# Kernel optimization log

Hardware: AMD Instinct MI355X
Metric: run time of the kernel (lower is better)

Reference implementation:

```python
import jax, jax.numpy as jnp
import numpy as np

B, K, D = 65536, 1024, 256
COMMITMENT_COST = 0.25


def setup_inputs() -> dict:
    key = jax.random.key(0)
    kz, kw = jax.random.split(key)
    z = jax.random.normal(kz, (B, D), dtype=jnp.float32)
    # torch init: uniform_(-1/num_embeddings, 1/num_embeddings)
    weight = jax.random.uniform(kw, (K, D), dtype=jnp.float32,
                                minval=-1.0 / K, maxval=1.0 / K)
    return {"z": z, "weight": weight}


def reference(z, weight):
    # squared L2 distances via expansion: ||z||^2 - 2 z.e + ||e||^2  -> [B, K]
    dists = (jnp.sum(z * z, axis=1, keepdims=True)
             - 2.0 * (z @ weight.T)
             + jnp.sum(weight * weight, axis=1))
    indices = jnp.argmin(dists, axis=1)          # [B]
    z_q = weight[indices]                         # [B, D] gather

    sg_z = jax.lax.stop_gradient(z)
    mse = jnp.mean((z_q - sg_z) ** 2)
    commitment_loss = COMMITMENT_COST * mse      # F.mse_loss(z.detach(), z_q)
    vq_loss = mse + commitment_loss              # F.mse_loss(z_q, z.detach()) + commitment

    # straight-through estimator
    z_q_st = z + jax.lax.stop_gradient(z_q - z)
    return z_q_st, vq_loss, indices
```

## Files before the change

### kernel.cpp

```cpp
#include <hip/hip_runtime.h>
#include <math.h>

#define B_N 65536
#define K_N 1024
#define D_N 256
#define CAPW 512
#define NWV 8

typedef __attribute__((ext_vector_type(8))) short bf16x8;
typedef __attribute__((ext_vector_type(4))) float f32x4;

__device__ __forceinline__ unsigned short f2bf(float f) {
    unsigned u = __float_as_uint(f);
    return (unsigned short)((u + 0x7FFFu + ((u >> 16) & 1u)) >> 16);
}
__device__ __forceinline__ unsigned encf(float f) {
    unsigned u = __float_as_uint(f);
    return u ^ ((unsigned)((int)u >> 31) | 0x80000000u);
}
__device__ __forceinline__ float decf(unsigned e) {
    unsigned u = (e & 0x80000000u) ? (e ^ 0x80000000u) : ~e;
    return __uint_as_float(u);
}
__device__ __forceinline__ void gload_lds16(const void* g, void* l) {
    __builtin_amdgcn_global_load_lds(
        (const __attribute__((address_space(1))) unsigned int*)g,
        (__attribute__((address_space(3))) unsigned int*)l, 16, 0, 0);
}

__device__ __forceinline__ float chain_dot(const float* __restrict__ zp,
                                           const float* __restrict__ wp) {
    float acc = 0.0f;
    #pragma unroll 1
    for (int j = 0; j < 64; ++j) {
        float4 za = *reinterpret_cast<const float4*>(zp + (j << 2));
        float4 wa = *reinterpret_cast<const float4*>(wp + (j << 2));
        acc = fmaf(za.x, wa.x, acc);
        acc = fmaf(za.y, wa.y, acc);
        acc = fmaf(za.z, wa.z, acc);
        acc = fmaf(za.w, wa.w, acc);
    }
    return acc;
}

__device__ __forceinline__ int pA(int i, int k) {
    return ((i + k) & 15) - 7 + 9 * ((k >> 4) & 1);
}
__device__ __forceinline__ int pB(int j, int k) {
    return ((j + 3 * k) & 15) - 7 + 5 * ((k >> 4) & 1);
}

__global__ void mfma_probe_kernel(int* __restrict__ flag) {
    const int l = threadIdx.x & 63;
    const int c15 = l & 15, g = l >> 4;
    bf16x8 afr[8], bfr[8];
    #pragma unroll
    for (int m = 0; m < 8; ++m)
        #pragma unroll
        for (int e = 0; e < 8; ++e) {
            const int k = m * 32 + g * 8 + e;
            afr[m][e] = (short)f2bf((float)pA(c15, k));
            bfr[m][e] = (short)f2bf((float)pB(c15, k));
        }
    f32x4 acc = {0.f, 0.f, 0.f, 0.f};
    #pragma unroll
    for (int m = 0; m < 8; ++m)
        acc = __builtin_amdgcn_mfma_f32_16x16x32_bf16(afr[m], bfr[m], acc, 0, 0, 0);
    int h1 = 1, h2 = 1;
    #pragma unroll 1
    for (int reg = 0; reg < 4; ++reg) {
        const int q = 4 * g + reg;
        int e1 = 0, e2 = 0;
        for (int k = 0; k < 32; ++k) {
            e1 += pA(q, k) * pB(c15, k);
            e2 += pA(c15, k) * pB(q, k);
        }
        e1 *= 8; e2 *= 8;
        if (acc[reg] != (float)e1) h1 = 0;
        if (acc[reg] != (float)e2) h2 = 0;
    }
    h1 = __all(h1); h2 = __all(h2);
    if (threadIdx.x == 0) *flag = h1 ? 0 : (h2 ? 1 : 2);
}

__global__ void wprep_kernel(const float* __restrict__ w,
                             float* __restrict__ ww,
                             unsigned short* __restrict__ wb) {
    int wave = (int)((blockIdx.x * blockDim.x + threadIdx.x) >> 6);
    int lane = threadIdx.x & 63;
    if (wave >= K_N) return;
    const float4 v = *reinterpret_cast<const float4*>(w + ((size_t)wave << 8) + (lane << 2));
    float s = v.x * v.x + v.y * v.y + v.z * v.z + v.w * v.w;
    #pragma unroll
    for (int off = 32; off; off >>= 1) s += __shfl_xor(s, off, 64);
    if (lane == 0) ww[wave] = s;
    ushort4 b;
    b.x = f2bf(v.x); b.y = f2bf(v.y); b.z = f2bf(v.z); b.w = f2bf(v.w);
    const int mp = lane >> 3;
    const int gp = (lane >> 1) & 3;
    const int hp = (wave >> 4) & 1;
    const size_t off_b = (size_t)(wave >> 5) * 16384
        + (size_t)(((hp * 8 + mp) * 64 + gp * 16 + (wave & 15)) * 16)
        + (size_t)((lane & 1) * 8);
    *reinterpret_cast<ushort4*>((char*)wb + off_b) = b;
}

__global__ __launch_bounds__(512, 4)
void vq_mfma_kernel(const float* __restrict__ z, const float* __restrict__ w,
                    const unsigned short* __restrict__ wb,
                    const float* __restrict__ ww,
                    const int* __restrict__ flagp,
                    float* __restrict__ zq_out,
                    float* __restrict__ idxf_out,
                    double* __restrict__ partial) {
    __shared__ alignas(16) short wbl[3][8192];
    __shared__ float wwlds[1024];
    __shared__ unsigned short rc[NWV][CAPW];
    __shared__ unsigned short dqv[NWV][CAPW];
    __shared__ float zz_l[NWV][16], band_l[NWV][16], thrm[NWV][16];
    __shared__ unsigned rowminU[NWV][16];
    __shared__ unsigned long long bestk[NWV][16];
    __shared__ double wsum[NWV];

    const int tid = threadIdx.x;
    const int wv = tid >> 6, l = tid & 63;
    const int c15 = l & 15, g = l >> 4;
    const int b0 = blockIdx.x << 7;
    const int rbase = b0 + (wv << 4);
    const int flag = flagp[0];
    const bool fb0 = !(flag == 0 || flag == 1);

#define STAGE(T, BUF) do {                                                    \
        const char* _s = (const char*)wb + (size_t)(T) * 16384 + tid * 16;    \
        char* _d = (char*)&wbl[BUF][0] + tid * 16;                            \
        gload_lds16(_s,         _d);                                          \
        gload_lds16(_s + 8192,  _d + 8192);                                   \
    } while (0)

    STAGE(0, 0);

    if (l < 16) {
        rowminU[wv][l] = 0xFFFFFFFFu;
        bestk[wv][l]   = ~0ull;
    }
    reinterpret_cast<float2*>(wwlds)[tid] = reinterpret_cast<const float2*>(ww)[tid];

    bool fbw = fb0;
    int n = 0;

    int ml[4], cl[4];
    #pragma unroll
    for (int reg = 0; reg < 4; ++reg) {
        if (flag == 1) { ml[reg] = c15;          cl[reg] = 4 * g + reg; }
        else           { ml[reg] = 4 * g + reg;  cl[reg] = c15;         }
    }

    bf16x8 afr[8];
    {
        const float* zr = z + ((size_t)(rbase + c15) << 8) + (g << 3);
        float s = 0.0f, a = 0.0f;
        #pragma unroll
        for (int m = 0; m < 8; ++m) {
            float4 lo = *reinterpret_cast<const float4*>(zr + (m << 5));
            float4 hi = *reinterpret_cast<const float4*>(zr + (m << 5) + 4);
            s += lo.x * lo.x + lo.y * lo.y + lo.z * lo.z + lo.w * lo.w;
            s += hi.x * hi.x + hi.y * hi.y + hi.z * hi.z + hi.w * hi.w;
            a += fabsf(lo.x) + fabsf(lo.y) + fabsf(lo.z) + fabsf(lo.w);
            a += fabsf(hi.x) + fabsf(hi.y) + fabsf(hi.z) + fabsf(hi.w);
            bf16x8 f;
            f[0] = (short)f2bf(lo.x); f[1] = (short)f2bf(lo.y);
            f[2] = (short)f2bf(lo.z); f[3] = (short)f2bf(lo.w);
            f[4] = (short)f2bf(hi.x); f[5] = (short)f2bf(hi.y);
            f[6] = (short)f2bf(hi.z); f[7] = (short)f2bf(hi.w);
            afr[m] = f;
        }
        s += __shfl_xor(s, 16, 64);
        s += __shfl_xor(s, 32, 64);
        a += __shfl_xor(a, 16, 64);
        a += __shfl_xor(a, 32, 64);
        if (g == 0) {
            zz_l[wv][c15]   = s;
            band_l[wv][c15] = a * 2.0e-5f + 1.0e-3f;
        }
    }

    STAGE(1, 1);

    __syncthreads();

    float zzv[4], bdv[4];
    #pragma unroll
    for (int reg = 0; reg < 4; ++reg) {
        zzv[reg] = zz_l[wv][ml[reg]];
        bdv[reg] = band_l[wv][ml[reg]];
    }

    float runmin[4] = {INFINITY, INFINITY, INFINITY, INFINITY};
    int base = 0;

#define ITER(C, CUR0, CUR1, PRV0, PRV1) do {                                  \
    if ((C) <= 32) {                                                          \
        if ((C) <= 30) {                                                      \
            const int _st = ((C) + 2 <= 31) ? ((C) + 2) : 0;                  \
            STAGE(_st, ((C) + 2) % 3);                                        \
        }                                                                     \
        const short* _sb = wbl[(C) % 3];                                      \
        CUR0 = (f32x4){0.f, 0.f, 0.f, 0.f};                                   \
        CUR1 = (f32x4){0.f, 0.f, 0.f, 0.f};                                   \
        _Pragma("unroll")                                                     \
        for (int m = 0; m < 8; ++m) {                                         \
            bf16x8 _b = *reinterpret_cast<const bf16x8*>(                     \
                &_sb[(m << 9) + (l << 3)]);                                   \
            CUR0 = __builtin_amdgcn_mfma_f32_16x16x32_bf16(afr[m], _b, CUR0, 0, 0, 0); \
        }                                                                     \
        _Pragma("unroll")                                                     \
        for (int m = 0; m < 8; ++m) {                                         \
            bf16x8 _b = *reinterpret_cast<const bf16x8*>(                     \
                &_sb[((8 + m) << 9) + (l << 3)]);                             \
            CUR1 = __builtin_amdgcn_mfma_f32_16x16x32_bf16(afr[m], _b, CUR1, 0, 0, 0); \
        }                                                                     \
    }                                                                         \
    if ((C) >= 1) {                                                           \
        const int _tc = ((C) <= 32) ? ((C) - 1) : 0;                          \
        const bool _docol = ((C) >= 2);                                       \
        const bool _dofm = ((C) <= 32);                                       \
        _Pragma("unroll")                                                     \
        for (int h = 0; h < 2; ++h) {                                         \
            const f32x4 _acc = h ? (PRV1) : (PRV0);                           \
            _Pragma("unroll")                                                 \
            for (int reg = 0; reg < 4; ++reg) {                               \
                const int _code = (_tc << 5) + (h << 4) + cl[reg];            \
                const float _dist = (zzv[reg] - 2.0f * _acc[reg]) + wwlds[_code]; \
                if (_docol) {                                                 \
                    const bool _pred = (_dist <= runmin[reg] + bdv[reg]);     \
                    const unsigned long long _mask = __ballot(_pred);         \
                    if (_mask) {                                              \
                        if (_pred) {                                          \
                            const int _slot = base + (int)__popcll(_mask & ((1ull << l) - 1ull)); \
                            if (_slot < CAPW) {                               \
                                rc[wv][_slot] = (unsigned short)((ml[reg] << 10) | _code); \
                                union { _Float16 h16; unsigned short u; } _cv; \
                                _cv.h16 = (_Float16)(_dist - zzv[reg]);       \
                                dqv[wv][_slot] = _cv.u;                       \
                            }                                                 \
                        }                                                     \
                        base += (int)__popcll(_mask);                         \
                    }                                                         \
                }                                                             \
                if (_dofm) runmin[reg] = fminf(runmin[reg], _dist);           \
            }                                                                 \
        }                                                                     \
        if (_dofm) {                                                          \
            if (flag == 1) {                                                  \
                _Pragma("unroll")                                             \
                for (int reg = 0; reg < 4; ++reg) {                           \
                    runmin[reg] = fminf(runmin[reg], __shfl_xor(runmin[reg], 16, 64)); \
                    runmin[reg] = fminf(runmin[reg], __shfl_xor(runmin[reg], 32, 64)); \
                }                                                             \
            } else {                                                          \
                _Pragma("unroll")                                             \
                for (int reg = 0; reg < 4; ++reg) {                           \
                    runmin[reg] = fminf(runmin[reg], __shfl_xor(runmin[reg], 1, 64)); \
                    runmin[reg] = fminf(runmin[reg], __shfl_xor(runmin[reg], 2, 64)); \
                    runmin[reg] = fminf(runmin[reg], __shfl_xor(runmin[reg], 4, 64)); \
                    runmin[reg] = fminf(runmin[reg], __shfl_xor(runmin[reg], 8, 64)); \
                }                                                             \
            }                                                                 \
        }                                                                     \
    }                                                                         \
    if ((C) <= 31) {                                                          \
        if ((C) <= 30) { asm volatile("s_waitcnt vmcnt(2) lgkmcnt(0)" ::: "memory"); } \
        else           { asm volatile("s_waitcnt vmcnt(0) lgkmcnt(0)" ::: "memory"); } \
        __builtin_amdgcn_sched_barrier(0);                                    \
        __builtin_amdgcn_s_barrier();                                         \
        __builtin_amdgcn_sched_barrier(0);                                    \
    }                                                                         \
} while (0)

    if (!fb0) {
        f32x4 aA0 = {0.f, 0.f, 0.f, 0.f}, aA1 = {0.f, 0.f, 0.f, 0.f};
        f32x4 aB0 = {0.f, 0.f, 0.f, 0.f}, aB1 = {0.f, 0.f, 0.f, 0.f};
        #pragma unroll 1
        for (int c = 0; c < 34; c += 2) {
            ITER(c,     aA0, aA1, aB0, aB1);
            ITER(c + 1, aB0, aB1, aA0, aA1);
        }

        n = base;
        if (n > CAPW) fbw = true;

        #pragma unroll
        for (int reg = 0; reg < 4; ++reg)
            atomicMin(&rowminU[wv][ml[reg]], encf(runmin[reg]));
        if (l < 16)
            thrm[wv][l] = (decf(rowminU[wv][l]) + band_l[wv][l]) - zz_l[wv][l] + 4.0e-4f;
    }
#undef ITER
#undef STAGE

    if (!fbw) {
        int viol = 0;
        #pragma unroll 1
        for (int i = l; i < n; i += 64) {
            const int e = rc[wv][i];
            const int m = e >> 10, code = e & 1023;
            union { _Float16 h16; unsigned short u; } cv;
            cv.u = dqv[wv][i];
            const float dval = (float)cv.h16;
            if (dval <= thrm[wv][m]) {
                const float dot = chain_dot(z + ((size_t)(rbase + m) << 8),
                                            w + ((size_t)code << 8));
                const float dist = (zz_l[wv][m] - 2.0f * dot) + wwlds[code];
                if (fabsf((dval + zz_l[wv][m]) - dist) > band_l[wv][m] + 4.0e-4f)
                    viol = 1;
                atomicMin(&bestk[wv][m],
                          ((unsigned long long)encf(dist) << 32) | (unsigned)code);
            }
        }
        if (__any(viol)) fbw = true;
    }
    if (fbw) {
        #pragma unroll 1
        for (int m = 0; m < 16; ++m) {
            const float zzm = zz_l[wv][m];
            const float* zp = z + ((size_t)(rbase + m) << 8);
            for (int code = l; code < 1024; code += 64) {
                const float dist = (zzm - 2.0f * chain_dot(zp, w + ((size_t)code << 8)))
                                 + wwlds[code];
                atomicMin(&bestk[wv][m],
                          ((unsigned long long)encf(dist) << 32) | (unsigned)code);
            }
        }
    }

    if (l < 16) {
        const int code = (int)(unsigned)(bestk[wv][l] & 0xFFFFFFFFull);
        idxf_out[rbase + l] = (float)code;
    }

    int codes[16];
    #pragma unroll
    for (int rr = 0; rr < 16; ++rr)
        codes[rr] = (int)(unsigned)(bestk[wv][rr] & 0xFFFFFFFFull);
    #pragma unroll 4
    for (int rr = 0; rr < 16; ++rr) {
        const float4 wv4 = *reinterpret_cast<const float4*>(
            w + ((size_t)codes[rr] << 8) + (l << 2));
        *reinterpret_cast<float4*>(
            zq_out + ((size_t)(rbase + rr) << 8) + (l << 2)) = wv4;
    }

    double s = 0.0;
    if (l < 16) s = (double)decf((unsigned)(bestk[wv][l] >> 32));
    #pragma unroll
    for (int off = 8; off; off >>= 1) s += __shfl_xor(s, off, 64);
    if (l == 0) wsum[wv] = s;
    __syncthreads();
    if (tid == 0) {
        double t = 0.0;
        #pragma unroll
        for (int i = 0; i < NWV; ++i) t += wsum[i];
        partial[blockIdx.x] = t;
    }
}

__global__ void finalize_loss_kernel(const double* __restrict__ partial,
                                     float* __restrict__ out) {
    __shared__ double sd[256];
    const int t = threadIdx.x;
    double s = 0.0;
    for (int i = t; i < 512; i += 256) s += partial[i];
    sd[t] = s;
    __syncthreads();
    #pragma unroll
    for (int off = 128; off; off >>= 1) {
        if (t < off) sd[t] += sd[t + off];
        __syncthreads();
    }
    if (t == 0) {
        double mse = sd[0] / ((double)B_N * (double)D_N);
        out[0] = (float)(mse * 1.25);
    }
}

extern "C" void kernel_launch(void* const* d_in, const int* in_sizes, int n_in,
                              void* d_out, int out_size, void* d_ws, size_t ws_size,
                              hipStream_t stream) {
    const float* z = (const float*)d_in[0];
    const float* w = (const float*)d_in[1];

    float* out  = (float*)d_out;
    float* zq   = out;
    float* loss = out + (size_t)B_N * D_N;
    float* idxf = loss + 1;

    char* wsb = (char*)d_ws;
    float*          ww      = (float*)(wsb);
    unsigned short* wb      = (unsigned short*)(wsb + 4096);
    int*            flag    = (int*)(wsb + 528384);
    double*         partial = (double*)(wsb + 528448);

    mfma_probe_kernel<<<1, 64, 0, stream>>>(flag);

    wprep_kernel<<<K_N / 4, 256, 0, stream>>>(w, ww, wb);

    vq_mfma_kernel<<<B_N / 128, 512, 0, stream>>>(z, w, wb, ww, flag,
                                                  zq, idxf, partial);

    finalize_loss_kernel<<<1, 256, 0, stream>>>(partial, loss);
}
```

Before: 167.4 us.

## Read codebook bf16 fragments directly from global memory instead of LDS staging

```diff
diff --git a/kernel.cpp b/kernel.cpp
--- a/kernel.cpp
+++ b/kernel.cpp
@@ -21,11 +21,6 @@
 __device__ __forceinline__ float decf(unsigned e) {
     unsigned u = (e & 0x80000000u) ? (e ^ 0x80000000u) : ~e;
     return __uint_as_float(u);
-}
-__device__ __forceinline__ void gload_lds16(const void* g, void* l) {
-    __builtin_amdgcn_global_load_lds(
-        (const __attribute__((address_space(1))) unsigned int*)g,
-        (__attribute__((address_space(3))) unsigned int*)l, 16, 0, 0);
 }
 
 __device__ __forceinline__ float chain_dot(const float* __restrict__ zp,
@@ -113,7 +108,6 @@
                     float* __restrict__ zq_out,
                     float* __restrict__ idxf_out,
                     double* __restrict__ partial) {
-    __shared__ alignas(16) short wbl[3][8192];
     __shared__ float wwlds[1024];
     __shared__ unsigned short rc[NWV][CAPW];
     __shared__ unsigned short dqv[NWV][CAPW];
@@ -129,15 +123,6 @@
     const int rbase = b0 + (wv << 4);
     const int flag = flagp[0];
     const bool fb0 = !(flag == 0 || flag == 1);
-
-#define STAGE(T, BUF) do {                                                    \
-        const char* _s = (const char*)wb + (size_t)(T) * 16384 + tid * 16;    \
-        char* _d = (char*)&wbl[BUF][0] + tid * 16;                            \
-        gload_lds16(_s,         _d);                                          \
-        gload_lds16(_s + 8192,  _d + 8192);                                   \
-    } while (0)
-
-    STAGE(0, 0);
 
     if (l < 16) {
         rowminU[wv][l] = 0xFFFFFFFFu;
@@ -184,8 +169,6 @@
         }
     }
 
-    STAGE(1, 1);
-
     __syncthreads();
 
     float zzv[4], bdv[4];
@@ -198,92 +181,83 @@
     float runmin[4] = {INFINITY, INFINITY, INFINITY, INFINITY};
     int base = 0;
 
-#define ITER(C, CUR0, CUR1, PRV0, PRV1) do {                                  \
-    if ((C) <= 32) {                                                          \
-        if ((C) <= 30) {                                                      \
-            const int _st = ((C) + 2 <= 31) ? ((C) + 2) : 0;                  \
-            STAGE(_st, ((C) + 2) % 3);                                        \
-        }                                                                     \
-        const short* _sb = wbl[(C) % 3];                                      \
-        CUR0 = (f32x4){0.f, 0.f, 0.f, 0.f};                                   \
-        CUR1 = (f32x4){0.f, 0.f, 0.f, 0.f};                                   \
-        _Pragma("unroll")                                                     \
-        for (int m = 0; m < 8; ++m) {                                         \
-            bf16x8 _b = *reinterpret_cast<const bf16x8*>(                     \
-                &_sb[(m << 9) + (l << 3)]);                                   \
-            CUR0 = __builtin_amdgcn_mfma_f32_16x16x32_bf16(afr[m], _b, CUR0, 0, 0, 0); \
-        }                                                                     \
-        _Pragma("unroll")                                                     \
-        for (int m = 0; m < 8; ++m) {                                         \
-            bf16x8 _b = *reinterpret_cast<const bf16x8*>(                     \
-                &_sb[((8 + m) << 9) + (l << 3)]);                             \
-            CUR1 = __builtin_amdgcn_mfma_f32_16x16x32_bf16(afr[m], _b, CUR1, 0, 0, 0); \
-        }                                                                     \
-    }                                                                         \
-    if ((C) >= 1) {                                                           \
-        const int _tc = ((C) <= 32) ? ((C) - 1) : 0;                          \
-        const bool _docol = ((C) >= 2);                                       \
-        const bool _dofm = ((C) <= 32);                                       \
-        _Pragma("unroll")                                                     \
-        for (int h = 0; h < 2; ++h) {                                         \
-            const f32x4 _acc = h ? (PRV1) : (PRV0);                           \
-            _Pragma("unroll")                                                 \
-            for (int reg = 0; reg < 4; ++reg) {                               \
-                const int _code = (_tc << 5) + (h << 4) + cl[reg];            \
-                const float _dist = (zzv[reg] - 2.0f * _acc[reg]) + wwlds[_code]; \
-                if (_docol) {                                                 \
-                    const bool _pred = (_dist <= runmin[reg] + bdv[reg]);     \
-                    const unsigned long long _mask = __ballot(_pred);         \
-                    if (_mask) {                                              \
-                        if (_pred) {                                          \
-                            const int _slot = base + (int)__popcll(_mask & ((1ull << l) - 1ull)); \
-                            if (_slot < CAPW) {                               \
-                                rc[wv][_slot] = (unsigned short)((ml[reg] << 10) | _code); \
-                                union { _Float16 h16; unsigned short u; } _cv; \
-                                _cv.h16 = (_Float16)(_dist - zzv[reg]);       \
-                                dqv[wv][_slot] = _cv.u;                       \
-                            }                                                 \
-                        }                                                     \
-                        base += (int)__popcll(_mask);                         \
+    const char* wbL = (const char*)wb + (l << 4);
+
+#define PROCESS(ACC, TC, DOCOL, DOFM)                                         \
+    _Pragma("unroll")                                                         \
+    for (int reg = 0; reg < 4; ++reg) {                                       \
+        const int _code = ((TC) << 5) + (h << 4) + cl[reg];                   \
+        const float _dist = (zzv[reg] - 2.0f * (ACC)[reg]) + wwlds[_code];    \
+        if (DOCOL) {                                                          \
+            const bool _pred = (_dist <= runmin[reg] + bdv[reg]);             \
+            const unsigned long long _mask = __ballot(_pred);                 \
+            if (_mask) {                                                      \
+                if (_pred) {                                                  \
+                    const int _slot = base + (int)__popcll(_mask & ((1ull << l) - 1ull)); \
+                    if (_slot < CAPW) {                                       \
+                        rc[wv][_slot] = (unsigned short)((ml[reg] << 10) | _code); \
+                        union { _Float16 h16; unsigned short u; } _cv;        \
+                        _cv.h16 = (_Float16)(_dist - zzv[reg]);               \
+                        dqv[wv][_slot] = _cv.u;                               \
                     }                                                         \
                 }                                                             \
-                if (_dofm) runmin[reg] = fminf(runmin[reg], _dist);           \
+                base += (int)__popcll(_mask);                                 \
             }                                                                 \
         }                                                                     \
-        if (_dofm) {                                                          \
-            if (flag == 1) {                                                  \
-                _Pragma("unroll")                                             \
-                for (int reg = 0; reg < 4; ++reg) {                           \
-                    runmin[reg] = fminf(runmin[reg], __shfl_xor(runmin[reg], 16, 64)); \
-                    runmin[reg] = fminf(runmin[reg], __shfl_xor(runmin[reg], 32, 64)); \
-                }                                                             \
-            } else {                                                          \
-                _Pragma("unroll")                                             \
-                for (int reg = 0; reg < 4; ++reg) {                           \
-                    runmin[reg] = fminf(runmin[reg], __shfl_xor(runmin[reg], 1, 64)); \
-                    runmin[reg] = fminf(runmin[reg], __shfl_xor(runmin[reg], 2, 64)); \
-                    runmin[reg] = fminf(runmin[reg], __shfl_xor(runmin[reg], 4, 64)); \
-                    runmin[reg] = fminf(runmin[reg], __shfl_xor(runmin[reg], 8, 64)); \
-                }                                                             \
-            }                                                                 \
+        if (DOFM) runmin[reg] = fminf(runmin[reg], _dist);                    \
+    }
+
+#define MINSYNC()                                                             \
+    if (flag == 1) {                                                          \
+        _Pragma("unroll")                                                     \
+        for (int reg = 0; reg < 4; ++reg) {                                   \
+            runmin[reg] = fminf(runmin[reg], __shfl_xor(runmin[reg], 16, 64)); \
+            runmin[reg] = fminf(runmin[reg], __shfl_xor(runmin[reg], 32, 64)); \
         }                                                                     \
-    }                                                                         \
-    if ((C) <= 31) {                                                          \
-        if ((C) <= 30) { asm volatile("s_waitcnt vmcnt(2) lgkmcnt(0)" ::: "memory"); } \
-        else           { asm volatile("s_waitcnt vmcnt(0) lgkmcnt(0)" ::: "memory"); } \
-        __builtin_amdgcn_sched_barrier(0);                                    \
-        __builtin_amdgcn_s_barrier();                                         \
-        __builtin_amdgcn_sched_barrier(0);                                    \
-    }                                                                         \
-} while (0)
+    } else {                                                                  \
+        _Pragma("unroll")                                                     \
+        for (int reg = 0; reg < 4; ++reg) {                                   \
+            runmin[reg] = fminf(runmin[reg], __shfl_xor(runmin[reg], 1, 64)); \
+            runmin[reg] = fminf(runmin[reg], __shfl_xor(runmin[reg], 2, 64)); \
+            runmin[reg] = fminf(runmin[reg], __shfl_xor(runmin[reg], 4, 64)); \
+            runmin[reg] = fminf(runmin[reg], __shfl_xor(runmin[reg], 8, 64)); \
+        }                                                                     \
+    }
 
     if (!fb0) {
-        f32x4 aA0 = {0.f, 0.f, 0.f, 0.f}, aA1 = {0.f, 0.f, 0.f, 0.f};
-        f32x4 aB0 = {0.f, 0.f, 0.f, 0.f}, aB1 = {0.f, 0.f, 0.f, 0.f};
         #pragma unroll 1
-        for (int c = 0; c < 34; c += 2) {
-            ITER(c,     aA0, aA1, aB0, aB1);
-            ITER(c + 1, aB0, aB1, aA0, aA1);
+        for (int t = 0; t < 32; ++t) {
+            const char* tp = wbL + t * 16384;
+            #pragma unroll
+            for (int h = 0; h < 2; ++h) {
+                bf16x8 bfr[8];
+                #pragma unroll
+                for (int m = 0; m < 8; ++m)
+                    bfr[m] = *reinterpret_cast<const bf16x8*>(tp + (h << 13) + (m << 10));
+                f32x4 acc = {0.f, 0.f, 0.f, 0.f};
+                #pragma unroll
+                for (int m = 0; m < 8; ++m)
+                    acc = __builtin_amdgcn_mfma_f32_16x16x32_bf16(afr[m], bfr[m], acc, 0, 0, 0);
+                if (t > 0) { PROCESS(acc, t, 1, 1) }
+                else       { PROCESS(acc, t, 0, 1) }
+            }
+            MINSYNC()
+        }
+
+        {
+            const char* tp = wbL;
+            #pragma unroll
+            for (int h = 0; h < 2; ++h) {
+                bf16x8 bfr[8];
+                #pragma unroll
+                for (int m = 0; m < 8; ++m)
+                    bfr[m] = *reinterpret_cast<const bf16x8*>(tp + (h << 13) + (m << 10));
+                f32x4 acc = {0.f, 0.f, 0.f, 0.f};
+                #pragma unroll
+                for (int m = 0; m < 8; ++m)
+                    acc = __builtin_amdgcn_mfma_f32_16x16x32_bf16(afr[m], bfr[m], acc, 0, 0, 0);
+                PROCESS(acc, 0, 1, 0)
+            }
         }
 
         n = base;
@@ -295,8 +269,8 @@
         if (l < 16)
             thrm[wv][l] = (decf(rowminU[wv][l]) + band_l[wv][l]) - zz_l[wv][l] + 4.0e-4f;
     }
-#undef ITER
-#undef STAGE
+#undef PROCESS
+#undef MINSYNC
 
     if (!fbw) {
         int viol = 0;
```

Result: slower. 188.9 us (+12.8%).

## Drop fp16 candidate distances and post-filter, reduce running-min every other tile

Applied to the files above, without the earlier changes.

```diff
diff --git a/kernel.cpp b/kernel.cpp
--- a/kernel.cpp
+++ b/kernel.cpp
@@ -4,7 +4,7 @@
 #define B_N 65536
 #define K_N 1024
 #define D_N 256
-#define CAPW 512
+#define CAPW 768
 #define NWV 8
 
 typedef __attribute__((ext_vector_type(8))) short bf16x8;
@@ -116,9 +116,7 @@
     __shared__ alignas(16) short wbl[3][8192];
     __shared__ float wwlds[1024];
     __shared__ unsigned short rc[NWV][CAPW];
-    __shared__ unsigned short dqv[NWV][CAPW];
-    __shared__ float zz_l[NWV][16], band_l[NWV][16], thrm[NWV][16];
-    __shared__ unsigned rowminU[NWV][16];
+    __shared__ float zz_l[NWV][16], band_l[NWV][16];
     __shared__ unsigned long long bestk[NWV][16];
     __shared__ double wsum[NWV];
 
@@ -139,10 +137,7 @@
 
     STAGE(0, 0);
 
-    if (l < 16) {
-        rowminU[wv][l] = 0xFFFFFFFFu;
-        bestk[wv][l]   = ~0ull;
-    }
+    if (l < 16) bestk[wv][l] = ~0ull;
     reinterpret_cast<float2*>(wwlds)[tid] = reinterpret_cast<const float2*>(ww)[tid];
 
     bool fbw = fb0;
@@ -237,12 +232,8 @@
                     if (_mask) {                                              \
                         if (_pred) {                                          \
                             const int _slot = base + (int)__popcll(_mask & ((1ull << l) - 1ull)); \
-                            if (_slot < CAPW) {                               \
+                            if (_slot < CAPW)                                 \
                                 rc[wv][_slot] = (unsigned short)((ml[reg] << 10) | _code); \
-                                union { _Float16 h16; unsigned short u; } _cv; \
-                                _cv.h16 = (_Float16)(_dist - zzv[reg]);       \
-                                dqv[wv][_slot] = _cv.u;                       \
-                            }                                                 \
                         }                                                     \
                         base += (int)__popcll(_mask);                         \
                     }                                                         \
@@ -250,7 +241,7 @@
                 if (_dofm) runmin[reg] = fminf(runmin[reg], _dist);           \
             }                                                                 \
         }                                                                     \
-        if (_dofm) {                                                          \
+        if (_dofm && (_tc & 1)) {                                             \
             if (flag == 1) {                                                  \
                 _Pragma("unroll")                                             \
                 for (int reg = 0; reg < 4; ++reg) {                           \
@@ -288,38 +279,22 @@
 
         n = base;
         if (n > CAPW) fbw = true;
-
-        #pragma unroll
-        for (int reg = 0; reg < 4; ++reg)
-            atomicMin(&rowminU[wv][ml[reg]], encf(runmin[reg]));
-        if (l < 16)
-            thrm[wv][l] = (decf(rowminU[wv][l]) + band_l[wv][l]) - zz_l[wv][l] + 4.0e-4f;
     }
 #undef ITER
 #undef STAGE
 
     if (!fbw) {
-        int viol = 0;
         #pragma unroll 1
         for (int i = l; i < n; i += 64) {
             const int e = rc[wv][i];
             const int m = e >> 10, code = e & 1023;
-            union { _Float16 h16; unsigned short u; } cv;
-            cv.u = dqv[wv][i];
-            const float dval = (float)cv.h16;
-            if (dval <= thrm[wv][m]) {
-                const float dot = chain_dot(z + ((size_t)(rbase + m) << 8),
-                                            w + ((size_t)code << 8));
-                const float dist = (zz_l[wv][m] - 2.0f * dot) + wwlds[code];
-                if (fabsf((dval + zz_l[wv][m]) - dist) > band_l[wv][m] + 4.0e-4f)
-                    viol = 1;
-                atomicMin(&bestk[wv][m],
-                          ((unsigned long long)encf(dist) << 32) | (unsigned)code);
-            }
-        }
-        if (__any(viol)) fbw = true;
-    }
-    if (fbw) {
+            const float dot = chain_dot(z + ((size_t)(rbase + m) << 8),
+                                        w + ((size_t)code << 8));
+            const float dist = (zz_l[wv][m] - 2.0f * dot) + wwlds[code];
+            atomicMin(&bestk[wv][m],
+                      ((unsigned long long)encf(dist) << 32) | (unsigned)code);
+        }
+    } else {
         #pragma unroll 1
         for (int m = 0; m < 16; ++m) {
             const float zzm = zz_l[wv][m];
```

Result: slower. 328.8 us (+96.5%).
